# Optimization experiments

Measured on AMD Instinct MI355X. Metric: run time of the kernel, lower is better.

The kernel has to match this reference:

```python
import jax, jax.numpy as jnp
import numpy as np

N = 50000      # nodes
E = 640000     # edges
F_IN = 64      # node feature dim
H = 128        # hidden channels
G = 256        # graphs in batch
NEG_SLOPE = 0.2
BN_EPS = 1e-5


def setup_inputs() -> dict:
    key = jax.random.key(0)
    ks = jax.random.split(key, 32)
    rn = lambda k, shape, s=0.1: jax.random.normal(k, shape, dtype=jnp.float32) * s
    inp = {
        'x': jax.random.normal(ks[0], (N, F_IN), dtype=jnp.float32),
        'edge_index': jax.random.randint(ks[1], (2, E), 0, N, dtype=jnp.int32),
        'batch': jnp.sort(jax.random.randint(ks[2], (N,), 0, G, dtype=jnp.int32)),
        # GATConv 1
        'W1': rn(ks[3], (F_IN, H)), 'as1': rn(ks[4], (H,)), 'ad1': rn(ks[5], (H,)), 'b1': jnp.zeros((H,), jnp.float32),
        # GATConv 2
        'W2': rn(ks[6], (H, H)), 'as2': rn(ks[7], (H,)), 'ad2': rn(ks[8], (H,)), 'b2': jnp.zeros((H,), jnp.float32),
        # GATConv 3
        'W3': rn(ks[9], (H, H)), 'as3': rn(ks[10], (H,)), 'ad3': rn(ks[11], (H,)), 'b3': jnp.zeros((H,), jnp.float32),
        # BatchNorm (inference: running stats)
        'g1': jnp.ones((H,), jnp.float32), 'be1': jnp.zeros((H,), jnp.float32), 'm1': rn(ks[12], (H,), 0.01), 'v1': jnp.ones((H,), jnp.float32),
        'g2': jnp.ones((H,), jnp.float32), 'be2': jnp.zeros((H,), jnp.float32), 'm2': rn(ks[13], (H,), 0.01), 'v2': jnp.ones((H,), jnp.float32),
        'g3': jnp.ones((H,), jnp.float32), 'be3': jnp.zeros((H,), jnp.float32), 'm3': rn(ks[14], (H,), 0.01), 'v3': jnp.ones((H,), jnp.float32),
        # MLP head
        'lw1': rn(ks[15], (H, H)), 'lb1': jnp.zeros((H,), jnp.float32),
        'lw2': rn(ks[16], (H, 1)), 'lb2': jnp.zeros((1,), jnp.float32),
    }
    return inp


def gat_layer(x, src, dst, W, a_src, a_dst, b, n):
    # PyG GATConv, heads=1: linear, per-edge attention, segment softmax over dst, scatter-add.
    h = x @ W                                  # [N, H]
    s_src = h @ a_src                          # [N]
    s_dst = h @ a_dst                          # [N]
    e = jax.nn.leaky_relu(s_src[src] + s_dst[dst], NEG_SLOPE)   # [E']
    m = jax.ops.segment_max(e, dst, num_segments=n)
    ex = jnp.exp(e - m[dst])
    denom = jax.ops.segment_sum(ex, dst, num_segments=n)
    coef = ex / denom[dst]                     # softmax per destination node
    out = jax.ops.segment_sum(coef[:, None] * h[src], dst, num_segments=n)
    return out + b


def batch_norm(x, g, b, mean, var):
    return (x - mean) * jax.lax.rsqrt(var + BN_EPS) * g + b


def reference(x, edge_index, batch,
              W1, as1, ad1, b1, W2, as2, ad2, b2, W3, as3, ad3, b3,
              g1, be1, m1, v1, g2, be2, m2, v2, g3, be3, m3, v3,
              lw1, lb1, lw2, lb2):
    n = x.shape[0]
    loops = jnp.arange(n, dtype=edge_index.dtype)      # PyG adds self-loops by default
    src = jnp.concatenate([edge_index[0], loops])
    dst = jnp.concatenate([edge_index[1], loops])

    h = gat_layer(x, src, dst, W1, as1, ad1, b1, n)
    h = jax.nn.relu(batch_norm(h, g1, be1, m1, v1))
    h = gat_layer(h, src, dst, W2, as2, ad2, b2, n)
    h = jax.nn.relu(batch_norm(h, g2, be2, m2, v2))
    h = gat_layer(h, src, dst, W3, as3, ad3, b3, n)
    h = jax.nn.relu(batch_norm(h, g3, be3, m3, v3))

    # global_mean_pool
    counts = jax.ops.segment_sum(jnp.ones((n,), h.dtype), batch, num_segments=G)
    pooled = jax.ops.segment_sum(h, batch, num_segments=G) / jnp.maximum(counts, 1.0)[:, None]

    out = jax.nn.relu(pooled @ lw1 + lb1)
    out = out @ lw2 + lb2                               # [G, 1]
    return out
```

## Files before the change

### kernel.cpp

```cpp
#include <hip/hip_runtime.h>

#define HD 128
#define NEG 0.2f
#define BNEPS 1e-5f

typedef unsigned int uint32;
typedef __attribute__((ext_vector_type(8))) short short8;
typedef __attribute__((ext_vector_type(4))) float floatx4;


__device__ inline float wave_max_f(float v) {
#pragma unroll
  for (int off = 32; off; off >>= 1) v = fmaxf(v, __shfl_xor(v, off, 64));
  return v;
}
__device__ inline float wave_sum_f(float v) {
#pragma unroll
  for (int off = 32; off; off >>= 1) v += __shfl_xor(v, off, 64);
  return v;
}
__device__ inline int wave_sum_i(int v) {
#pragma unroll
  for (int off = 32; off; off >>= 1) v += __shfl_xor(v, off, 64);
  return v;
}
__device__ inline int wave_iscan_i(int v, int lane) {
#pragma unroll
  for (int off = 1; off < 64; off <<= 1) {
    int t = __shfl_up(v, off, 64);
    if (lane >= off) v += t;
  }
  return v;
}
__device__ inline uint32 f2bf(float f) {
  uint32 u = __float_as_uint(f);
  return (u + 0x7fffu + ((u >> 16) & 1u)) >> 16;
}


__global__ void k_init_deg(int* __restrict__ deg, int n) {
  int i = blockIdx.x * blockDim.x + threadIdx.x;
  if (i < n) deg[i] = 1;
}

__global__ void k_hist(const int* __restrict__ dst, int* __restrict__ deg, int E) {
  int i = blockIdx.x * blockDim.x + threadIdx.x;
  if (i < E) atomicAdd(&deg[dst[i]], 1);
}

__global__ __launch_bounds__(256) void k_scan_part(const int* __restrict__ deg,
                                                   int* __restrict__ part, int n) {
  const int t = threadIdx.x, lane = t & 63, wave = t >> 6;
  const int i = blockIdx.x * 256 + t;
  int v = (i < n) ? deg[i] : 0;
  int wv = wave_sum_i(v);
  __shared__ int ws[4];
  if (lane == 0) ws[wave] = wv;
  __syncthreads();
  if (t == 0) part[blockIdx.x] = ws[0] + ws[1] + ws[2] + ws[3];
}

__global__ __launch_bounds__(256) void k_scan_part2(int* __restrict__ part, int nb) {
  const int t = threadIdx.x, lane = t & 63, wave = t >> 6;
  int v = (t < nb) ? part[t] : 0;
  int x = wave_iscan_i(v, lane);
  __shared__ int ws[4];
  if (lane == 63) ws[wave] = x;
  __syncthreads();
  int add = 0;
#pragma unroll
  for (int w = 0; w < 4; ++w)
    if (w < wave) add += ws[w];
  x += add;
  if (t < nb) part[t] = x;
}

__global__ __launch_bounds__(256) void k_scan_final(const int* __restrict__ deg,
                                                    const int* __restrict__ part,
                                                    int* __restrict__ offs, int n) {
  const int t = threadIdx.x, lane = t & 63, wave = t >> 6;
  const int b = blockIdx.x;
  const int i = b * 256 + t;
  int v = (i < n) ? deg[i] : 0;
  int x = wave_iscan_i(v, lane);
  __shared__ int ws[4];
  if (lane == 63) ws[wave] = x;
  __syncthreads();
  int add = (b > 0) ? part[b - 1] : 0;
#pragma unroll
  for (int w = 0; w < 4; ++w)
    if (w < wave) add += ws[w];
  x += add;
  if (i < n) offs[i + 1] = x;
  if (i == 0) offs[0] = 0;
}

__global__ void k_fill_self(const int* __restrict__ offs, int* __restrict__ csr,
                            int* __restrict__ cursor, int n) {
  int i = blockIdx.x * blockDim.x + threadIdx.x;
  if (i < n) { int o = offs[i]; csr[o] = i; cursor[i] = o + 1; }
}

__global__ void k_fill_edges(const int* __restrict__ src, const int* __restrict__ dst,
                             int* __restrict__ cursor, int* __restrict__ csr, int E) {
  int i = blockIdx.x * blockDim.x + threadIdx.x;
  if (i < E) { int p = atomicAdd(&cursor[dst[i]], 1); csr[p] = src[i]; }
}

template <int K>
__global__ __launch_bounds__(256) void k_packw(const float* __restrict__ W,
                                               uint32* __restrict__ PW) {
  const int idx = blockIdx.x * 256 + threadIdx.x;
  const int total = 8 * (K / 32) * 64 * 4;
  if (idx >= total) return;
  const int e2 = idx & 3;
  const int l = (idx >> 2) & 63;
  const int f = idx >> 8;
  const int kc = f % (K / 32), ct = f / (K / 32);
  const int k0 = kc * 32 + (l >> 4) * 8 + e2 * 2;
  const int col = ct * 16 + (l & 15);
  const float w0 = W[k0 * HD + col], w1 = W[(k0 + 1) * HD + col];
  PW[idx] = f2bf(w0) | (f2bf(w1) << 16);
}

template <int K>
__global__ __launch_bounds__(256)
void k_gemm_mfma(const float* __restrict__ X, const uint32* __restrict__ PW,
                 const float* __restrict__ a_s, const float* __restrict__ a_d,
                 uint32* __restrict__ Hh, float* __restrict__ ssrc,
                 float* __restrict__ sdst, int n) {
  constexpr int KC = K / 32;
  __shared__ uint32 Xl[64 * K / 2];
  __shared__ float sred[4][64][2];
  const int t = threadIdx.x;
  const int wv = t >> 6, l = t & 63;
  const int rowbase = blockIdx.x * 64;

  short8 bfr[2][KC];
#pragma unroll
  for (int c2 = 0; c2 < 2; ++c2)
#pragma unroll
    for (int kc = 0; kc < KC; ++kc) {
      const int f = (wv * 2 + c2) * KC + kc;
      bfr[c2][kc] = *((const short8*)PW + f * 64 + l);
    }

  {
    const int PAIRS = 64 * K / 2;
    for (int i = t; i < PAIRS; i += 256) {
      const int row = i / (K / 2), kp = i % (K / 2);
      const int r = min(rowbase + row, n - 1);
      const float2 v = *(const float2*)&X[(long)r * K + kp * 2];
      const uint32 p = f2bf(v.x) | (f2bf(v.y) << 16);
      int byte = row * (K * 2) + kp * 4;
      byte ^= (row & 7) << 4;
      Xl[byte >> 2] = p;
    }
  }
  __syncthreads();

  floatx4 acc[4][2];
#pragma unroll
  for (int rt = 0; rt < 4; ++rt) {
    acc[rt][0] = (floatx4){0.f, 0.f, 0.f, 0.f};
    acc[rt][1] = (floatx4){0.f, 0.f, 0.f, 0.f};
  }
  const int row_l = l & 15, kgrp = l >> 4;
#pragma unroll
  for (int rt = 0; rt < 4; ++rt) {
    const int row = rt * 16 + row_l;
#pragma unroll
    for (int kc = 0; kc < KC; ++kc) {
      const int byte = (row * (K * 2) + kc * 64 + kgrp * 16) ^ ((row & 7) << 4);
      const short8 af = *(const short8*)((const char*)Xl + byte);
      acc[rt][0] = __builtin_amdgcn_mfma_f32_16x16x32_bf16(af, bfr[0][kc], acc[rt][0], 0, 0, 0);
      acc[rt][1] = __builtin_amdgcn_mfma_f32_16x16x32_bf16(af, bfr[1][kc], acc[rt][1], 0, 0, 0);
    }
  }

  const int j0 = wv * 32 + (l & 15);
  const float as0 = a_s[j0], as1 = a_s[j0 + 16];
  const float ad0 = a_d[j0], ad1 = a_d[j0 + 16];
#pragma unroll
  for (int rt = 0; rt < 4; ++rt) {
#pragma unroll
    for (int r = 0; r < 4; ++r) {
      const float v0 = acc[rt][0][r], v1 = acc[rt][1][r];
      float ps = v0 * as0 + v1 * as1;
      float pd = v0 * ad0 + v1 * ad1;
#pragma unroll
      for (int m = 1; m < 16; m <<= 1) {
        ps += __shfl_xor(ps, m, 64);
        pd += __shfl_xor(pd, m, 64);
      }
      const int rowl = rt * 16 + (l >> 4) * 4 + r;
      if ((l & 15) == 0) {
        sred[wv][rowl][0] = ps;
        sred[wv][rowl][1] = pd;
      }
      const int R = rowbase + rowl;
      if (R < n) Hh[(long)R * 64 + wv * 16 + (l & 15)] = f2bf(v0) | (f2bf(v1) << 16);
    }
  }
  __syncthreads();
  if (t < 64) {
    const int R = rowbase + t;
    if (R < n) {
      ssrc[R] = sred[0][t][0] + sred[1][t][0] + sred[2][t][0] + sred[3][t][0];
      sdst[R] = sred[0][t][1] + sred[1][t][1] + sred[2][t][1] + sred[3][t][1];
    }
  }
}

__global__ __launch_bounds__(256)
void k_agg(const uint32* __restrict__ Hh, const float* __restrict__ ssrc,
           const float* __restrict__ sdst, const int* __restrict__ offs,
           const int* __restrict__ csr, const float* __restrict__ bias,
           const float* __restrict__ gam, const float* __restrict__ bet,
           const float* __restrict__ mu, const float* __restrict__ var,
           float* __restrict__ Y, int n) {
  const int wid = (blockIdx.x * blockDim.x + threadIdx.x) >> 6;
  const int lane = threadIdx.x & 63;
  if (wid >= n) return;
  const int s0 = offs[wid], s1 = offs[wid + 1];
  const float sdv = sdst[wid];
  const int c0 = (lane >> 4) * 32 + (lane & 15);
  const int c1 = c0 + 16;
  float acc0 = 0.f, acc1 = 0.f, denom = 0.f, mx = -1e30f;
  for (int base = s0; base < s1; base += 64) {
    const int m = min(64, s1 - base);
    int sidx = 0;
    float e = -1e30f;
    if (lane < m) {
      sidx = csr[base + lane];
      float tt = ssrc[sidx] + sdv;
      e = (tt > 0.f) ? tt : NEG * tt;
    }
    const float cmx = wave_max_f(e);
    const float nmx = fmaxf(mx, cmx);
    if (nmx > mx) {
      const float sc = __expf(mx - nmx);
      acc0 *= sc; acc1 *= sc; denom *= sc;
      mx = nmx;
    }
    const float p = (lane < m) ? __expf(e - mx) : 0.f;
    denom += wave_sum_f(p);
    int jj = 0;
    for (; jj + 8 <= m; jj += 8) {
      const int i0 = __builtin_amdgcn_readlane(sidx, jj + 0);
      const int i1 = __builtin_amdgcn_readlane(sidx, jj + 1);
      const int i2 = __builtin_amdgcn_readlane(sidx, jj + 2);
      const int i3 = __builtin_amdgcn_readlane(sidx, jj + 3);
      const int i4 = __builtin_amdgcn_readlane(sidx, jj + 4);
      const int i5 = __builtin_amdgcn_readlane(sidx, jj + 5);
      const int i6 = __builtin_amdgcn_readlane(sidx, jj + 6);
      const int i7 = __builtin_amdgcn_readlane(sidx, jj + 7);
      const uint32 pu = __float_as_uint(p);
      const float w0 = __uint_as_float(__builtin_amdgcn_readlane(pu, jj + 0));
      const float w1 = __uint_as_float(__builtin_amdgcn_readlane(pu, jj + 1));
      const float w2 = __uint_as_float(__builtin_amdgcn_readlane(pu, jj + 2));
      const float w3 = __uint_as_float(__builtin_amdgcn_readlane(pu, jj + 3));
      const float w4 = __uint_as_float(__builtin_amdgcn_readlane(pu, jj + 4));
      const float w5 = __uint_as_float(__builtin_amdgcn_readlane(pu, jj + 5));
      const float w6 = __uint_as_float(__builtin_amdgcn_readlane(pu, jj + 6));
      const float w7 = __uint_as_float(__builtin_amdgcn_readlane(pu, jj + 7));
      const uint32 g0 = Hh[i0 * 64 + lane];
      const uint32 g1 = Hh[i1 * 64 + lane];
      const uint32 g2 = Hh[i2 * 64 + lane];
      const uint32 g3 = Hh[i3 * 64 + lane];
      const uint32 g4 = Hh[i4 * 64 + lane];
      const uint32 g5 = Hh[i5 * 64 + lane];
      const uint32 g6 = Hh[i6 * 64 + lane];
      const uint32 g7 = Hh[i7 * 64 + lane];
      acc0 = fmaf(w0, __uint_as_float(g0 << 16), acc0);
      acc1 = fmaf(w0, __uint_as_float(g0 & 0xffff0000u), acc1);
      acc0 = fmaf(w1, __uint_as_float(g1 << 16), acc0);
      acc1 = fmaf(w1, __uint_as_float(g1 & 0xffff0000u), acc1);
      acc0 = fmaf(w2, __uint_as_float(g2 << 16), acc0);
      acc1 = fmaf(w2, __uint_as_float(g2 & 0xffff0000u), acc1);
      acc0 = fmaf(w3, __uint_as_float(g3 << 16), acc0);
      acc1 = fmaf(w3, __uint_as_float(g3 & 0xffff0000u), acc1);
      acc0 = fmaf(w4, __uint_as_float(g4 << 16), acc0);
      acc1 = fmaf(w4, __uint_as_float(g4 & 0xffff0000u), acc1);
      acc0 = fmaf(w5, __uint_as_float(g5 << 16), acc0);
      acc1 = fmaf(w5, __uint_as_float(g5 & 0xffff0000u), acc1);
      acc0 = fmaf(w6, __uint_as_float(g6 << 16), acc0);
      acc1 = fmaf(w6, __uint_as_float(g6 & 0xffff0000u), acc1);
      acc0 = fmaf(w7, __uint_as_float(g7 << 16), acc0);
      acc1 = fmaf(w7, __uint_as_float(g7 & 0xffff0000u), acc1);
    }
    for (; jj < m; ++jj) {
      const int s = __builtin_amdgcn_readlane(sidx, jj);
      const float w =
          __uint_as_float(__builtin_amdgcn_readlane(__float_as_uint(p), jj));
      const uint32 gv = Hh[s * 64 + lane];
      acc0 = fmaf(w, __uint_as_float(gv << 16), acc0);
      acc1 = fmaf(w, __uint_as_float(gv & 0xffff0000u), acc1);
    }
  }
  const float inv = 1.f / denom;
  float v0 = acc0 * inv + bias[c0];
  float v1 = acc1 * inv + bias[c1];
  const float sc0 = gam[c0] * rsqrtf(var[c0] + BNEPS);
  const float sc1 = gam[c1] * rsqrtf(var[c1] + BNEPS);
  v0 = fmaxf((v0 - mu[c0]) * sc0 + bet[c0], 0.f);
  v1 = fmaxf((v1 - mu[c1]) * sc1 + bet[c1], 0.f);
  Y[(long)wid * HD + c0] = v0;
  Y[(long)wid * HD + c1] = v1;
}

__global__ __launch_bounds__(256)
void k_pool_head(const float* __restrict__ Y, const int* __restrict__ batch, int n,
                 const float* __restrict__ lw1, const float* __restrict__ lb1,
                 const float* __restrict__ lw2, const float* __restrict__ lb2,
                 float* __restrict__ out) {
  const int g = blockIdx.x;
  const int wave = threadIdx.x >> 6, lane = threadIdx.x & 63;
  int lo = 0, hi = n;
  while (lo < hi) { int mid = (lo + hi) >> 1; if (batch[mid] < g) lo = mid + 1; else hi = mid; }
  const int start = lo;
  hi = n;
  while (lo < hi) { int mid = (lo + hi) >> 1; if (batch[mid] < g + 1) lo = mid + 1; else hi = mid; }
  const int end = lo;
  const int c0 = lane * 2;
  float m0 = 0.f, m1 = 0.f;
  for (int i = start + wave; i < end; i += 4) {
    float2 hv = *(const float2*)&Y[(long)i * HD + c0];
    m0 += hv.x;
    m1 += hv.y;
  }
  __shared__ float red[4][HD];
  red[wave][c0] = m0;
  red[wave][c0 + 1] = m1;
  __syncthreads();
  if (wave == 0) {
    m0 = red[0][c0] + red[1][c0] + red[2][c0] + red[3][c0];
    m1 = red[0][c0 + 1] + red[1][c0 + 1] + red[2][c0 + 1] + red[3][c0 + 1];
    const float cnt = (float)(end - start);
    const float invc = (cnt > 0.f) ? 1.f / cnt : 0.f;
    m0 *= invc;
    m1 *= invc;
    float t0 = lb1[c0], t1 = lb1[c0 + 1];
    for (int k = 0; k < HD; ++k) {
      float pv = __shfl((k & 1) ? m1 : m0, k >> 1, 64);
      float2 w2 = *(const float2*)&lw1[k * HD + c0];
      t0 = fmaf(pv, w2.x, t0);
      t1 = fmaf(pv, w2.y, t1);
    }
    t0 = fmaxf(t0, 0.f);
    t1 = fmaxf(t1, 0.f);
    float p = t0 * lw2[c0] + t1 * lw2[c0 + 1];
#pragma unroll
    for (int off = 32; off; off >>= 1) p += __shfl_xor(p, off, 64);
    if (lane == 0) out[g] = p + lb2[0];
  }
}


extern "C" void kernel_launch(void* const* d_in, const int* in_sizes, int n_in,
                              void* d_out, int out_size, void* d_ws, size_t ws_size,
                              hipStream_t stream) {
  const float* x = (const float*)d_in[0];
  const int* ei = (const int*)d_in[1];
  const int* batch = (const int*)d_in[2];
  const float* W1 = (const float*)d_in[3];
  const float* as1 = (const float*)d_in[4];
  const float* ad1 = (const float*)d_in[5];
  const float* b1 = (const float*)d_in[6];
  const float* W2 = (const float*)d_in[7];
  const float* as2 = (const float*)d_in[8];
  const float* ad2 = (const float*)d_in[9];
  const float* b2 = (const float*)d_in[10];
  const float* W3 = (const float*)d_in[11];
  const float* as3 = (const float*)d_in[12];
  const float* ad3 = (const float*)d_in[13];
  const float* b3 = (const float*)d_in[14];
  const float* g1 = (const float*)d_in[15];
  const float* be1 = (const float*)d_in[16];
  const float* m1 = (const float*)d_in[17];
  const float* v1 = (const float*)d_in[18];
  const float* g2 = (const float*)d_in[19];
  const float* be2 = (const float*)d_in[20];
  const float* m2 = (const float*)d_in[21];
  const float* v2 = (const float*)d_in[22];
  const float* g3 = (const float*)d_in[23];
  const float* be3 = (const float*)d_in[24];
  const float* m3 = (const float*)d_in[25];
  const float* v3 = (const float*)d_in[26];
  const float* lw1 = (const float*)d_in[27];
  const float* lb1 = (const float*)d_in[28];
  const float* lw2 = (const float*)d_in[29];
  const float* lb2 = (const float*)d_in[30];

  const int n = in_sizes[0] / 64;
  const int E = in_sizes[1] / 2;
  const int* src = ei;
  const int* dst = ei + E;

  uint32* hbuf = (uint32*)d_ws;
  float* ybuf = (float*)(hbuf + (long)n * 64);
  float* ssrc = ybuf + (long)n * HD;
  float* sdstv = ssrc + n;
  int* deg = (int*)(sdstv + n);
  int* offs = deg + n;
  int* cursor = offs + n + 1;
  int* csr = cursor + n;
  int* part = csr + (E + n);
  uint32* PW1 = (uint32*)(part + 256);
  uint32* PW2 = PW1 + 8192;
  uint32* PW3 = PW2 + 8192;

  const int B = 256;
  dim3 blk(B);
  const int nb = (n + B - 1) / B;

  k_packw<64><<<dim3(16), blk, 0, stream>>>(W1, PW1);
  k_packw<128><<<dim3(32), blk, 0, stream>>>(W2, PW2);
  k_packw<128><<<dim3(32), blk, 0, stream>>>(W3, PW3);

  k_init_deg<<<dim3(nb), blk, 0, stream>>>(deg, n);
  k_hist<<<dim3((E + B - 1) / B), blk, 0, stream>>>(dst, deg, E);
  k_scan_part<<<dim3(nb), blk, 0, stream>>>(deg, part, n);
  k_scan_part2<<<dim3(1), blk, 0, stream>>>(part, nb);
  k_scan_final<<<dim3(nb), blk, 0, stream>>>(deg, part, offs, n);
  k_fill_self<<<dim3(nb), blk, 0, stream>>>(offs, csr, cursor, n);
  k_fill_edges<<<dim3((E + B - 1) / B), blk, 0, stream>>>(src, dst, cursor, csr, E);

  const dim3 ggrid((n + 63) / 64);
  const dim3 agrid((n + 3) / 4);

  k_gemm_mfma<64><<<ggrid, blk, 0, stream>>>(x, PW1, as1, ad1, hbuf, ssrc, sdstv, n);
  k_agg<<<agrid, blk, 0, stream>>>(hbuf, ssrc, sdstv, offs, csr, b1, g1, be1, m1, v1, ybuf, n);
  k_gemm_mfma<128><<<ggrid, blk, 0, stream>>>(ybuf, PW2, as2, ad2, hbuf, ssrc, sdstv, n);
  k_agg<<<agrid, blk, 0, stream>>>(hbuf, ssrc, sdstv, offs, csr, b2, g2, be2, m2, v2, ybuf, n);
  k_gemm_mfma<128><<<ggrid, blk, 0, stream>>>(ybuf, PW3, as3, ad3, hbuf, ssrc, sdstv, n);
  k_agg<<<agrid, blk, 0, stream>>>(hbuf, ssrc, sdstv, offs, csr, b3, g3, be3, m3, v3, ybuf, n);

  k_pool_head<<<dim3(256), blk, 0, stream>>>(ybuf, batch, n, lw1, lb1, lw2, lb2,
                                             (float*)d_out);
}
```

Measured before the change: 268.1 us.

## Store activations in bf16, fold attention vectors into weights, merge setup kernels

The aggregation output is now written as packed bf16 instead of fp32. It is loaded directly into LDS by the next GEMM, and the weight packing uses a k-permutation that matches the packed layout. The attention scores are computed as an extra MFMA against precomputed W·a_src and W·a_dst vectors, which replaces the per-row shuffle reductions and the LDS reduction. The weight-pack kernels are merged into one launch, and the self-loop CSR fill is folded into the scan. Together these cut activation memory traffic and launch count. The cost is extra bf16 rounding of the activations and of the folded attention vectors.

Result: faster. 252.7 us (-5.8%).

```diff
diff --git a/kernel.cpp b/kernel.cpp
--- a/kernel.cpp
+++ b/kernel.cpp
@@ -35,6 +35,16 @@
 __device__ inline uint32 f2bf(float f) {
   uint32 u = __float_as_uint(f);
   return (u + 0x7fffu + ((u >> 16) & 1u)) >> 16;
+}
+__device__ inline void kpair(int kc, int lg, int e2, bool perm, int& k_lo, int& k_hi) {
+  if (!perm) {
+    k_lo = kc * 32 + lg * 8 + e2 * 2;
+    k_hi = k_lo + 1;
+  } else {
+    int w = kc * 16 + lg * 4 + e2;
+    k_lo = ((w >> 4) << 5) + (w & 15);
+    k_hi = k_lo + 16;
+  }
 }
 
 
@@ -77,7 +87,9 @@
 
 __global__ __launch_bounds__(256) void k_scan_final(const int* __restrict__ deg,
                                                     const int* __restrict__ part,
-                                                    int* __restrict__ offs, int n) {
+                                                    int* __restrict__ offs,
+                                                    int* __restrict__ csr,
+                                                    int* __restrict__ cursor, int n) {
   const int t = threadIdx.x, lane = t & 63, wave = t >> 6;
   const int b = blockIdx.x;
   const int i = b * 256 + t;
@@ -91,14 +103,13 @@
   for (int w = 0; w < 4; ++w)
     if (w < wave) add += ws[w];
   x += add;
-  if (i < n) offs[i + 1] = x;
+  if (i < n) {
+    const int excl = x - v;
+    offs[i + 1] = x;
+    csr[excl] = i;
+    cursor[i] = excl + 1;
+  }
   if (i == 0) offs[0] = 0;
-}
-
-__global__ void k_fill_self(const int* __restrict__ offs, int* __restrict__ csr,
-                            int* __restrict__ cursor, int n) {
-  int i = blockIdx.x * blockDim.x + threadIdx.x;
-  if (i < n) { int o = offs[i]; csr[o] = i; cursor[i] = o + 1; }
 }
 
 __global__ void k_fill_edges(const int* __restrict__ src, const int* __restrict__ dst,
@@ -107,31 +118,71 @@
   if (i < E) { int p = atomicAdd(&cursor[dst[i]], 1); csr[p] = src[i]; }
 }
 
-template <int K>
-__global__ __launch_bounds__(256) void k_packw(const float* __restrict__ W,
-                                               uint32* __restrict__ PW) {
-  const int idx = blockIdx.x * 256 + threadIdx.x;
-  const int total = 8 * (K / 32) * 64 * 4;
-  if (idx >= total) return;
-  const int e2 = idx & 3;
-  const int l = (idx >> 2) & 63;
-  const int f = idx >> 8;
-  const int kc = f % (K / 32), ct = f / (K / 32);
-  const int k0 = kc * 32 + (l >> 4) * 8 + e2 * 2;
-  const int col = ct * 16 + (l & 15);
-  const float w0 = W[k0 * HD + col], w1 = W[(k0 + 1) * HD + col];
-  PW[idx] = f2bf(w0) | (f2bf(w1) << 16);
-}
-
-template <int K>
 __global__ __launch_bounds__(256)
-void k_gemm_mfma(const float* __restrict__ X, const uint32* __restrict__ PW,
-                 const float* __restrict__ a_s, const float* __restrict__ a_d,
-                 uint32* __restrict__ Hh, float* __restrict__ ssrc,
-                 float* __restrict__ sdst, int n) {
+void k_pack(const float* __restrict__ W1, const float* __restrict__ as1v,
+            const float* __restrict__ ad1v, const float* __restrict__ W2,
+            const float* __restrict__ as2v, const float* __restrict__ ad2v,
+            const float* __restrict__ W3, const float* __restrict__ as3v,
+            const float* __restrict__ ad3v, uint32* __restrict__ PW1,
+            uint32* __restrict__ PW2, uint32* __restrict__ PW3,
+            uint32* __restrict__ BFA1, uint32* __restrict__ BFA2,
+            uint32* __restrict__ BFA3) {
+  const int b = blockIdx.x, t = threadIdx.x;
+  if (b < 80) {
+    const float* W;
+    uint32* PW;
+    int KC, local;
+    bool perm;
+    if (b < 16) { W = W1; PW = PW1; KC = 2; perm = false; local = b; }
+    else if (b < 48) { W = W2; PW = PW2; KC = 4; perm = true; local = b - 16; }
+    else { W = W3; PW = PW3; KC = 4; perm = true; local = b - 48; }
+    const int idx = local * 256 + t;
+    const int e2 = idx & 3, l = (idx >> 2) & 63, f = idx >> 8;
+    const int kc = f % KC, ct = f / KC;
+    int k_lo, k_hi;
+    kpair(kc, l >> 4, e2, perm, k_lo, k_hi);
+    const int col = ct * 16 + (l & 15);
+    PW[idx] = f2bf(W[k_lo * HD + col]) | (f2bf(W[k_hi * HD + col]) << 16);
+  } else {
+    const int layer = b - 80;
+    const float* W = layer == 0 ? W1 : layer == 1 ? W2 : W3;
+    const float* av = layer == 0 ? as1v : layer == 1 ? as2v : as3v;
+    const float* dv = layer == 0 ? ad1v : layer == 1 ? ad2v : ad3v;
+    uint32* BFA = layer == 0 ? BFA1 : layer == 1 ? BFA2 : BFA3;
+    const int K = layer == 0 ? 64 : 128, KC = K / 32;
+    const bool perm = layer != 0;
+    __shared__ float ws[128], wd[128];
+    if (t < K) {
+      float s = 0.f, d = 0.f;
+      for (int j = 0; j < HD; ++j) {
+        const float w = W[t * HD + j];
+        s = fmaf(w, av[j], s);
+        d = fmaf(w, dv[j], d);
+      }
+      ws[t] = s;
+      wd[t] = d;
+    }
+    __syncthreads();
+    const int total = KC * 256;
+    for (int idx = t; idx < total; idx += 256) {
+      const int e2 = idx & 3, l = (idx >> 2) & 63, kc = idx >> 8;
+      int k_lo, k_hi;
+      kpair(kc, l >> 4, e2, perm, k_lo, k_hi);
+      const int li = l & 15;
+      const float lo = li == 0 ? ws[k_lo] : li == 1 ? wd[k_lo] : 0.f;
+      const float hi = li == 0 ? ws[k_hi] : li == 1 ? wd[k_hi] : 0.f;
+      BFA[idx] = f2bf(lo) | (f2bf(hi) << 16);
+    }
+  }
+}
+
+template <int K, bool BF16IN>
+__global__ __launch_bounds__(256)
+void k_gemm_mfma(const void* __restrict__ Xv, const uint32* __restrict__ PW,
+                 const uint32* __restrict__ BFA, uint32* __restrict__ Hh,
+                 float* __restrict__ ssrc, float* __restrict__ sdst, int n) {
   constexpr int KC = K / 32;
   __shared__ uint32 Xl[64 * K / 2];
-  __shared__ float sred[4][64][2];
   const int t = threadIdx.x;
   const int wv = t >> 6, l = t & 63;
   const int rowbase = blockIdx.x * 64;
@@ -140,30 +191,43 @@
 #pragma unroll
   for (int c2 = 0; c2 < 2; ++c2)
 #pragma unroll
-    for (int kc = 0; kc < KC; ++kc) {
-      const int f = (wv * 2 + c2) * KC + kc;
-      bfr[c2][kc] = *((const short8*)PW + f * 64 + l);
-    }
-
-  {
+    for (int kc = 0; kc < KC; ++kc)
+      bfr[c2][kc] = *((const short8*)PW + ((wv * 2 + c2) * KC + kc) * 64 + l);
+  short8 bfa[KC];
+  if (wv == 0) {
+#pragma unroll
+    for (int kc = 0; kc < KC; ++kc) bfa[kc] = *((const short8*)BFA + kc * 64 + l);
+  }
+
+  if (BF16IN) {
+    const uint32* Xb = (const uint32*)Xv;
+#pragma unroll
+    for (int B = t; B < 64 * (K / 8); B += 256) {
+      const int row = B / (K / 8), cb = B % (K / 8);
+      const int r = min(rowbase + row, n - 1);
+      const uint4 v = *(const uint4*)&Xb[(long)r * (K / 2) + cb * 4];
+      *(uint4*)&Xl[row * (K / 2) + (cb ^ (row & 7)) * 4] = v;
+    }
+  } else {
+    const float* X = (const float*)Xv;
     const int PAIRS = 64 * K / 2;
     for (int i = t; i < PAIRS; i += 256) {
       const int row = i / (K / 2), kp = i % (K / 2);
       const int r = min(rowbase + row, n - 1);
       const float2 v = *(const float2*)&X[(long)r * K + kp * 2];
-      const uint32 p = f2bf(v.x) | (f2bf(v.y) << 16);
       int byte = row * (K * 2) + kp * 4;
       byte ^= (row & 7) << 4;
-      Xl[byte >> 2] = p;
+      Xl[byte >> 2] = f2bf(v.x) | (f2bf(v.y) << 16);
     }
   }
   __syncthreads();
 
-  floatx4 acc[4][2];
+  floatx4 acc[4][2], acc2[4];
 #pragma unroll
   for (int rt = 0; rt < 4; ++rt) {
     acc[rt][0] = (floatx4){0.f, 0.f, 0.f, 0.f};
     acc[rt][1] = (floatx4){0.f, 0.f, 0.f, 0.f};
+    acc2[rt] = (floatx4){0.f, 0.f, 0.f, 0.f};
   }
   const int row_l = l & 15, kgrp = l >> 4;
 #pragma unroll
@@ -175,40 +239,30 @@
       const short8 af = *(const short8*)((const char*)Xl + byte);
       acc[rt][0] = __builtin_amdgcn_mfma_f32_16x16x32_bf16(af, bfr[0][kc], acc[rt][0], 0, 0, 0);
       acc[rt][1] = __builtin_amdgcn_mfma_f32_16x16x32_bf16(af, bfr[1][kc], acc[rt][1], 0, 0, 0);
-    }
-  }
-
-  const int j0 = wv * 32 + (l & 15);
-  const float as0 = a_s[j0], as1 = a_s[j0 + 16];
-  const float ad0 = a_d[j0], ad1 = a_d[j0 + 16];
+      if (wv == 0)
+        acc2[rt] = __builtin_amdgcn_mfma_f32_16x16x32_bf16(af, bfa[kc], acc2[rt], 0, 0, 0);
+    }
+  }
+
 #pragma unroll
   for (int rt = 0; rt < 4; ++rt) {
 #pragma unroll
     for (int r = 0; r < 4; ++r) {
-      const float v0 = acc[rt][0][r], v1 = acc[rt][1][r];
-      float ps = v0 * as0 + v1 * as1;
-      float pd = v0 * ad0 + v1 * ad1;
-#pragma unroll
-      for (int m = 1; m < 16; m <<= 1) {
-        ps += __shfl_xor(ps, m, 64);
-        pd += __shfl_xor(pd, m, 64);
+      const int R = rowbase + rt * 16 + kgrp * 4 + r;
+      if (R < n)
+        Hh[(long)R * 64 + wv * 16 + row_l] =
+            f2bf(acc[rt][0][r]) | (f2bf(acc[rt][1][r]) << 16);
+    }
+  }
+  if (wv == 0 && row_l < 2) {
+    float* tgt = (row_l == 0) ? ssrc : sdst;
+#pragma unroll
+    for (int rt = 0; rt < 4; ++rt)
+#pragma unroll
+      for (int r = 0; r < 4; ++r) {
+        const int R = rowbase + rt * 16 + kgrp * 4 + r;
+        if (R < n) tgt[R] = acc2[rt][r];
       }
-      const int rowl = rt * 16 + (l >> 4) * 4 + r;
-      if ((l & 15) == 0) {
-        sred[wv][rowl][0] = ps;
-        sred[wv][rowl][1] = pd;
-      }
-      const int R = rowbase + rowl;
-      if (R < n) Hh[(long)R * 64 + wv * 16 + (l & 15)] = f2bf(v0) | (f2bf(v1) << 16);
-    }
-  }
-  __syncthreads();
-  if (t < 64) {
-    const int R = rowbase + t;
-    if (R < n) {
-      ssrc[R] = sred[0][t][0] + sred[1][t][0] + sred[2][t][0] + sred[3][t][0];
-      sdst[R] = sred[0][t][1] + sred[1][t][1] + sred[2][t][1] + sred[3][t][1];
-    }
   }
 }
 
@@ -218,7 +272,7 @@
            const int* __restrict__ csr, const float* __restrict__ bias,
            const float* __restrict__ gam, const float* __restrict__ bet,
            const float* __restrict__ mu, const float* __restrict__ var,
-           float* __restrict__ Y, int n) {
+           uint32* __restrict__ Ybf, int n) {
   const int wid = (blockIdx.x * blockDim.x + threadIdx.x) >> 6;
   const int lane = threadIdx.x & 63;
   if (wid >= n) return;
@@ -305,12 +359,11 @@
   const float sc1 = gam[c1] * rsqrtf(var[c1] + BNEPS);
   v0 = fmaxf((v0 - mu[c0]) * sc0 + bet[c0], 0.f);
   v1 = fmaxf((v1 - mu[c1]) * sc1 + bet[c1], 0.f);
-  Y[(long)wid * HD + c0] = v0;
-  Y[(long)wid * HD + c1] = v1;
+  Ybf[(long)wid * 64 + lane] = f2bf(v0) | (f2bf(v1) << 16);
 }
 
 __global__ __launch_bounds__(256)
-void k_pool_head(const float* __restrict__ Y, const int* __restrict__ batch, int n,
+void k_pool_head(const uint32* __restrict__ Ybf, const int* __restrict__ batch, int n,
                  const float* __restrict__ lw1, const float* __restrict__ lb1,
                  const float* __restrict__ lw2, const float* __restrict__ lb2,
                  float* __restrict__ out) {
@@ -322,34 +375,35 @@
   hi = n;
   while (lo < hi) { int mid = (lo + hi) >> 1; if (batch[mid] < g + 1) lo = mid + 1; else hi = mid; }
   const int end = lo;
-  const int c0 = lane * 2;
+  const int c0 = (lane >> 4) * 32 + (lane & 15);
+  const int c1 = c0 + 16;
   float m0 = 0.f, m1 = 0.f;
   for (int i = start + wave; i < end; i += 4) {
-    float2 hv = *(const float2*)&Y[(long)i * HD + c0];
-    m0 += hv.x;
-    m1 += hv.y;
+    const uint32 gv = Ybf[(long)i * 64 + lane];
+    m0 += __uint_as_float(gv << 16);
+    m1 += __uint_as_float(gv & 0xffff0000u);
   }
   __shared__ float red[4][HD];
   red[wave][c0] = m0;
-  red[wave][c0 + 1] = m1;
+  red[wave][c1] = m1;
   __syncthreads();
   if (wave == 0) {
     m0 = red[0][c0] + red[1][c0] + red[2][c0] + red[3][c0];
-    m1 = red[0][c0 + 1] + red[1][c0 + 1] + red[2][c0 + 1] + red[3][c0 + 1];
+    m1 = red[0][c1] + red[1][c1] + red[2][c1] + red[3][c1];
     const float cnt = (float)(end - start);
     const float invc = (cnt > 0.f) ? 1.f / cnt : 0.f;
     m0 *= invc;
     m1 *= invc;
-    float t0 = lb1[c0], t1 = lb1[c0 + 1];
+    float t0 = lb1[c0], t1 = lb1[c1];
     for (int k = 0; k < HD; ++k) {
-      float pv = __shfl((k & 1) ? m1 : m0, k >> 1, 64);
-      float2 w2 = *(const float2*)&lw1[k * HD + c0];
-      t0 = fmaf(pv, w2.x, t0);
-      t1 = fmaf(pv, w2.y, t1);
+      const int srcl = ((k >> 5) << 4) + (k & 15);
+      const float pv = __shfl(((k >> 4) & 1) ? m1 : m0, srcl, 64);
+      t0 = fmaf(pv, lw1[k * HD + c0], t0);
+      t1 = fmaf(pv, lw1[k * HD + c1], t1);
     }
     t0 = fmaxf(t0, 0.f);
     t1 = fmaxf(t1, 0.f);
-    float p = t0 * lw2[c0] + t1 * lw2[c0 + 1];
+    float p = t0 * lw2[c0] + t1 * lw2[c1];
 #pragma unroll
     for (int off = 32; off; off >>= 1) p += __shfl_xor(p, off, 64);
     if (lane == 0) out[g] = p + lb2[0];
@@ -398,8 +452,8 @@
   const int* dst = ei + E;
 
   uint32* hbuf = (uint32*)d_ws;
-  float* ybuf = (float*)(hbuf + (long)n * 64);
-  float* ssrc = ybuf + (long)n * HD;
+  uint32* ybuf = hbuf + (long)n * 64;
+  float* ssrc = (float*)(ybuf + (long)n * 64);
   float* sdstv = ssrc + n;
   int* deg = (int*)(sdstv + n);
   int* offs = deg + n;
@@ -407,33 +461,34 @@
   int* csr = cursor + n;
   int* part = csr + (E + n);
   uint32* PW1 = (uint32*)(part + 256);
-  uint32* PW2 = PW1 + 8192;
+  uint32* PW2 = PW1 + 4096;
   uint32* PW3 = PW2 + 8192;
+  uint32* BFA1 = PW3 + 8192;
+  uint32* BFA2 = BFA1 + 512;
+  uint32* BFA3 = BFA2 + 1024;
 
   const int B = 256;
   dim3 blk(B);
   const int nb = (n + B - 1) / B;
 
-  k_packw<64><<<dim3(16), blk, 0, stream>>>(W1, PW1);
-  k_packw<128><<<dim3(32), blk, 0, stream>>>(W2, PW2);
-  k_packw<128><<<dim3(32), blk, 0, stream>>>(W3, PW3);
+  k_pack<<<dim3(83), blk, 0, stream>>>(W1, as1, ad1, W2, as2, ad2, W3, as3, ad3,
+                                       PW1, PW2, PW3, BFA1, BFA2, BFA3);
 
   k_init_deg<<<dim3(nb), blk, 0, stream>>>(deg, n);
   k_hist<<<dim3((E + B - 1) / B), blk, 0, stream>>>(dst, deg, E);
   k_scan_part<<<dim3(nb), blk, 0, stream>>>(deg, part, n);
   k_scan_part2<<<dim3(1), blk, 0, stream>>>(part, nb);
-  k_scan_final<<<dim3(nb), blk, 0, stream>>>(deg, part, offs, n);
-  k_fill_self<<<dim3(nb), blk, 0, stream>>>(offs, csr, cursor, n);
+  k_scan_final<<<dim3(nb), blk, 0, stream>>>(deg, part, offs, csr, cursor, n);
   k_fill_edges<<<dim3((E + B - 1) / B), blk, 0, stream>>>(src, dst, cursor, csr, E);
 
   const dim3 ggrid((n + 63) / 64);
   const dim3 agrid((n + 3) / 4);
 
-  k_gemm_mfma<64><<<ggrid, blk, 0, stream>>>(x, PW1, as1, ad1, hbuf, ssrc, sdstv, n);
+  k_gemm_mfma<64, false><<<ggrid, blk, 0, stream>>>(x, PW1, BFA1, hbuf, ssrc, sdstv, n);
   k_agg<<<agrid, blk, 0, stream>>>(hbuf, ssrc, sdstv, offs, csr, b1, g1, be1, m1, v1, ybuf, n);
-  k_gemm_mfma<128><<<ggrid, blk, 0, stream>>>(ybuf, PW2, as2, ad2, hbuf, ssrc, sdstv, n);
+  k_gemm_mfma<128, true><<<ggrid, blk, 0, stream>>>(ybuf, PW2, BFA2, hbuf, ssrc, sdstv, n);
   k_agg<<<agrid, blk, 0, stream>>>(hbuf, ssrc, sdstv, offs, csr, b2, g2, be2, m2, v2, ybuf, n);
-  k_gemm_mfma<128><<<ggrid, blk, 0, stream>>>(ybuf, PW3, as3, ad3, hbuf, ssrc, sdstv, n);
+  k_gemm_mfma<128, true><<<ggrid, blk, 0, stream>>>(ybuf, PW3, BFA3, hbuf, ssrc, sdstv, n);
   k_agg<<<agrid, blk, 0, stream>>>(hbuf, ssrc, sdstv, offs, csr, b3, g3, be3, m3, v3, ybuf, n);
 
   k_pool_head<<<dim3(256), blk, 0, stream>>>(ybuf, batch, n, lw1, lb1, lw2, lb2,
```
